# Optimization experiments

Hardware: AMD Instinct MI355X
Metric: run time of the kernel (lower is better)

The kernel has to match this reference:

```python
import jax, jax.numpy as jnp
import numpy as np

NUM_NODES = 100000
NUM_REL = 237
D = 200            # entity_out_dim_1 * nheads_GAT_1 = 100*2
C = 50             # conv_out_channels
B = 8192           # batch of (h, r, t) triples


def setup_inputs() -> dict:
    key = jax.random.key(0)
    ks = jax.random.split(key, 8)
    heads = jax.random.randint(ks[0], (B, 1), 0, NUM_NODES)
    rels = jax.random.randint(ks[1], (B, 1), 0, NUM_REL)
    tails = jax.random.randint(ks[2], (B, 1), 0, NUM_NODES)
    batch_inputs = jnp.concatenate([heads, rels, tails], axis=1).astype(jnp.int64)
    return {
        "batch_inputs": batch_inputs,
        "final_entity_embeddings": jax.random.normal(ks[3], (NUM_NODES, D), jnp.float32),
        "final_relation_embeddings": jax.random.normal(ks[4], (NUM_REL, D), jnp.float32),
        "W_ent2rel": jax.random.normal(ks[5], (NUM_REL, D, D), jnp.float32) * (1.0 / np.sqrt(D)),
        "conv_w": jax.random.normal(ks[6], (C, 3), jnp.float32) * 0.5,
        "conv_b": jnp.zeros((C,), jnp.float32),
        "fc_w": jax.random.normal(ks[7], (1, C * D), jnp.float32) * (1.0 / np.sqrt(C * D)),
        "fc_b": jnp.zeros((1,), jnp.float32),
    }


def reference(batch_inputs, final_entity_embeddings, final_relation_embeddings,
              W_ent2rel, conv_w, conv_b, fc_w, fc_b):
    h_idx, r_idx, t_idx = batch_inputs[:, 0], batch_inputs[:, 1], batch_inputs[:, 2]
    src = final_entity_embeddings[h_idx]        # [B, D]
    rel = final_relation_embeddings[r_idx]      # [B, D]
    tail = final_entity_embeddings[t_idx]       # [B, D]
    W = W_ent2rel[r_idx]                        # [B, D, D] per-edge relation transform
    # bmm([B,1,D], [B,D,D]) -> [B,1,D], nonlinearity_ent2rel = tanh
    src = jnp.tanh(jnp.einsum('bd,bde->be', src, W))
    tail = jnp.tanh(jnp.einsum('bd,bde->be', tail, W))
    # ConvKB: stack triple as length-3 sequence, Conv2d kernel (1,3) over seq
    stacked = jnp.stack([src, rel, tail], axis=1)            # [B, 3, D]
    conv = jnp.einsum('bkd,ck->bcd', stacked, conv_w) + conv_b[None, :, None]
    conv = jax.nn.relu(conv)                                  # dropout p=0.0 (eval)
    flat = conv.reshape(conv.shape[0], -1)                    # [B, C*D] (C-major, matches torch view)
    out = flat @ fc_w.T + fc_b                                # [B, 1]
    return out
```

## Files before the change

kernel.cpp:

```cpp
#include <hip/hip_runtime.h>
#include <hip/hip_bf16.h>
#include <math.h>

#define DDIM 200
#define D4   50
#define CCH  50
#define NREL 237
#define MAXE 8
#define AROWS 16
#define NT   256
#define KT   7
#define KTKG 28
#define NCOLP 208
#define OSTRIDE 204
#define PACK_UNITS (NREL * KTKG * NCOLP)

typedef __attribute__((ext_vector_type(8))) short bf16x8;
typedef __attribute__((ext_vector_type(4))) float f32x4;

__device__ __forceinline__ uint f2bf(float x) {
    __hip_bfloat16 h = __float2bfloat16(x);
    return (uint)*reinterpret_cast<ushort*>(&h);
}
__device__ __forceinline__ float fast_tanh(float x) {
    const float xc = fminf(fmaxf(x, -20.f), 20.f);
    const float e  = __expf(2.f * xc);
    return 1.f - __fdividef(2.f, e + 1.f);
}

__global__ __launch_bounds__(1024) void prep_kernel(
    const float* __restrict__ W, ushort* __restrict__ Wpk, int do_pack,
    const int* __restrict__ bi, int B, int nblk,
    int* __restrict__ perm, int* __restrict__ blk_r,
    int* __restrict__ blk_start, int* __restrict__ blk_cnt,
    int* __restrict__ eidArr)
{
    const int tid = threadIdx.x;

    if (blockIdx.x != 0) {
        if (!do_pack) return;
        const int u = (blockIdx.x - 1) * 1024 + tid;
        if (u >= PACK_UNITS) return;
        const int col  = u % NCOLP;
        const int rk   = u / NCOLP;
        const int ktkg = rk % KTKG;
        const int r    = rk / KTKG;
        const int k0   = ktkg * 8;
        uint4 pk = {0u, 0u, 0u, 0u};
        if (col < DDIM) {
            const float* base = W + (size_t)r * DDIM * DDIM + col;
            uint vv[8];
            #pragma unroll
            for (int j = 0; j < 8; ++j) {
                const int k = k0 + j;
                vv[j] = (k < DDIM) ? f2bf(base[(size_t)k * DDIM]) : 0u;
            }
            pk.x = vv[0] | (vv[1] << 16);
            pk.y = vv[2] | (vv[3] << 16);
            pk.z = vv[4] | (vv[5] << 16);
            pk.w = vv[6] | (vv[7] << 16);
        }
        *(uint4*)&Wpk[(size_t)u * 8] = pk;
        return;
    }

    __shared__ int hist[NREL];
    __shared__ int offs[NREL];
    __shared__ int wsum[16], wsum2[16];
    const int lane = tid & 63;
    const int w    = tid >> 6;

    if (tid < NREL) hist[tid] = 0;
    __syncthreads();
    for (int i = tid; i < B; i += 1024)
        atomicAdd(&hist[bi[i * 3 + 1]], 1);
    __syncthreads();

    const int v  = (tid < NREL) ? hist[tid] : 0;
    const int v2 = (tid < NREL) ? (v + MAXE - 1) / MAXE : 0;
    int s = v, s2 = v2;
    #pragma unroll
    for (int off = 1; off < 64; off <<= 1) {
        const int u  = __shfl_up(s,  off, 64);
        const int u2 = __shfl_up(s2, off, 64);
        if (lane >= off) { s += u; s2 += u2; }
    }
    if (lane == 63) { wsum[w] = s; wsum2[w] = s2; }
    __syncthreads();
    int base = 0, base2 = 0;
    for (int i = 0; i < w; ++i) { base += wsum[i]; base2 += wsum2[i]; }
    const int my_off  = base  + s  - v;
    const int my_boff = base2 + s2 - v2;
    if (tid < NREL) offs[tid] = my_off;
    __syncthreads();

    for (int i = tid; i < nblk; i += 1024) blk_cnt[i] = 0;
    if (tid < NREL && v > 0) {
        const int nb = (v + MAXE - 1) / MAXE;
        const int cb = v / nb, ext = v - cb * nb;
        int pos = my_off;
        for (int j = 0; j < nb; ++j) {
            const int c = cb + (j < ext ? 1 : 0);
            blk_r[my_boff + j]     = tid;
            blk_start[my_boff + j] = pos;
            blk_cnt[my_boff + j]   = c;
            pos += c;
        }
    }
    __syncthreads();
    for (int i = tid; i < B; i += 1024) {
        const int pos = atomicAdd(&offs[bi[i * 3 + 1]], 1);
        perm[pos] = i;
    }
    __syncthreads();
    for (int p = tid; p < B; p += 1024) {
        const int b = perm[p];
        eidArr[2 * p]     = bi[3 * b + 0];
        eidArr[2 * p + 1] = bi[3 * b + 2];
    }
}

template <bool PACKED>
__global__ __launch_bounds__(NT) void spkbgat_mfma_kernel(
    const float*  __restrict__ ent,
    const float*  __restrict__ rel_emb,
    const float*  __restrict__ W,
    const ushort* __restrict__ Wpk,
    const float*  __restrict__ conv_w,
    const float*  __restrict__ conv_b,
    const float*  __restrict__ fc_w,
    const float*  __restrict__ fc_b,
    const int*    __restrict__ perm,
    const int*    __restrict__ blk_r,
    const int*    __restrict__ blk_start,
    const int*    __restrict__ blk_cnt,
    const int*    __restrict__ eidArr,
    int nblk,
    float*        __restrict__ out)
{
    __shared__ __align__(16) ushort Ash[KTKG * AROWS * 8];
    __shared__ __align__(16) float  Osh[AROWS][OSTRIDE];
    __shared__ __align__(16) float4 rl4[D4];
    __shared__ __align__(16) float  cwb[CCH][4];

    const int tid  = threadIdx.x;
    const int w    = tid >> 6;
    const int lane = tid & 63;
    const int l16  = lane & 15;
    const int kg   = lane >> 4;

    const int bid = blockIdx.x;
    const int q = nblk >> 3, rmd = nblk & 7;
    const int xcd = bid & 7, idx = bid >> 3;
    const int gidx = (xcd < rmd ? xcd * (q + 1) : rmd * (q + 1) + (xcd - rmd) * q) + idx;

    const int cnt = blk_cnt[gidx];
    if (cnt == 0) return;

    const int r     = blk_r[gidx];
    const int start = blk_start[gidx];
    const int rows  = 2 * cnt;

    if (tid < CCH) {
        cwb[tid][0] = conv_w[tid * 3 + 0];
        cwb[tid][1] = conv_w[tid * 3 + 1];
        cwb[tid][2] = conv_w[tid * 3 + 2];
        cwb[tid][3] = conv_b[tid];
    }
    if (tid < D4) rl4[tid] = ((const float4*)rel_emb)[r * D4 + tid];

    for (int u = tid; u < KTKG * AROWS; u += NT) {
        const int row  = u & (AROWS - 1);
        const int ktkg = u >> 4;
        uint4 pk = {0u, 0u, 0u, 0u};
        if (ktkg < 25 && row < rows) {
            const int eid = eidArr[2 * start + row];
            const float* xp = ent + (size_t)eid * DDIM + ktkg * 8;
            const float4 x0 = *(const float4*)xp;
            const float4 x1 = *(const float4*)(xp + 4);
            pk.x = f2bf(x0.x) | (f2bf(x0.y) << 16);
            pk.y = f2bf(x0.z) | (f2bf(x0.w) << 16);
            pk.z = f2bf(x1.x) | (f2bf(x1.y) << 16);
            pk.w = f2bf(x1.z) | (f2bf(x1.w) << 16);
        }
        *(uint4*)&Ash[u * 8] = pk;
    }
    __syncthreads();

    const int nslots = (w == 0) ? 4 : 3;
    const float*  __restrict__ Wr = W + (size_t)r * DDIM * DDIM;
    const ushort* __restrict__ Wp0 = Wpk + (size_t)r * KTKG * NCOLP * 8
                                   + ((size_t)kg * NCOLP) * 8 + (size_t)l16 * 8;

    bf16x8 a_frag[KT];
    #pragma unroll
    for (int kt = 0; kt < KT; ++kt)
        a_frag[kt] = *(const bf16x8*)&Ash[((kt * 4 + kg) * AROWS + l16) * 8];

    f32x4 acc[4];
    #pragma unroll
    for (int s = 0; s < 4; ++s) acc[s] = (f32x4){0.f, 0.f, 0.f, 0.f};

    if (PACKED) {
        bf16x8 bcur[4], bnxt[4];
        #pragma unroll
        for (int s = 0; s < 4; ++s)
            if (s < nslots)
                bcur[s] = *(const bf16x8*)(Wp0 + (size_t)(w + 4 * s) * 16 * 8);
        #pragma unroll
        for (int kt = 0; kt < KT; ++kt) {
            if (kt + 1 < KT) {
                const ushort* pn = Wp0 + (size_t)(kt + 1) * 4 * NCOLP * 8;
                #pragma unroll
                for (int s = 0; s < 4; ++s)
                    if (s < nslots)
                        bnxt[s] = *(const bf16x8*)(pn + (size_t)(w + 4 * s) * 16 * 8);
            }
            #pragma unroll
            for (int s = 0; s < 4; ++s)
                if (s < nslots)
                    acc[s] = __builtin_amdgcn_mfma_f32_16x16x32_bf16(
                        a_frag[kt], bcur[s], acc[s], 0, 0, 0);
            #pragma unroll
            for (int s = 0; s < 4; ++s)
                if (s < nslots) bcur[s] = bnxt[s];
        }
    } else {
        for (int kt = 0; kt < KT; ++kt) {
            const int k0b = (kt * 4 + kg) * 8;
            #pragma unroll
            for (int s = 0; s < 4; ++s) {
                if (s < nslots) {
                    const int col = (w + 4 * s) * 16 + l16;
                    bf16x8 bfr;
                    #pragma unroll
                    for (int j = 0; j < 8; ++j) {
                        const int k = k0b + j;
                        const float vv = (k < DDIM && col < DDIM) ? Wr[k * DDIM + col] : 0.f;
                        bfr[j] = (short)f2bf(vv);
                    }
                    acc[s] = __builtin_amdgcn_mfma_f32_16x16x32_bf16(
                        a_frag[kt], bfr, acc[s], 0, 0, 0);
                }
            }
        }
    }

    #pragma unroll
    for (int s = 0; s < 4; ++s) {
        if (s < nslots) {
            const int gcol = (w + 4 * s) * 16 + l16;
            if (gcol < DDIM) {
                #pragma unroll
                for (int v = 0; v < 4; ++v) {
                    const int grow = kg * 4 + v;
                    if (grow < rows)
                        Osh[grow][gcol] = fast_tanh(acc[s][v]);
                }
            }
        }
    }
    __syncthreads();

    float4 sa[2] = {{0,0,0,0}, {0,0,0,0}};
    if (lane < D4) {
        const float4 rv = rl4[lane];
        float4 se[2], te[2];
        #pragma unroll
        for (int s2 = 0; s2 < 2; ++s2) {
            const int e = w + 4 * s2;
            if (e < cnt) {
                se[s2] = *(const float4*)&Osh[2 * e][4 * lane];
                te[s2] = *(const float4*)&Osh[2 * e + 1][4 * lane];
            } else {
                se[s2] = (float4){0,0,0,0};
                te[s2] = (float4){0,0,0,0};
            }
        }
        for (int c = 0; c < CCH; ++c) {
            const float4 cw  = *(const float4*)&cwb[c][0];
            const float4 fc4 = ((const float4*)fc_w)[c * D4 + lane];
            #pragma unroll
            for (int s2 = 0; s2 < 2; ++s2) {
                const float v0 = fmaf(cw.x, se[s2].x, fmaf(cw.y, rv.x, fmaf(cw.z, te[s2].x, cw.w)));
                const float v1 = fmaf(cw.x, se[s2].y, fmaf(cw.y, rv.y, fmaf(cw.z, te[s2].y, cw.w)));
                const float v2 = fmaf(cw.x, se[s2].z, fmaf(cw.y, rv.z, fmaf(cw.z, te[s2].z, cw.w)));
                const float v3 = fmaf(cw.x, se[s2].w, fmaf(cw.y, rv.w, fmaf(cw.z, te[s2].w, cw.w)));
                sa[s2].x = fmaf(fmaxf(v0, 0.f), fc4.x, sa[s2].x);
                sa[s2].y = fmaf(fmaxf(v1, 0.f), fc4.y, sa[s2].y);
                sa[s2].z = fmaf(fmaxf(v2, 0.f), fc4.z, sa[s2].z);
                sa[s2].w = fmaf(fmaxf(v3, 0.f), fc4.w, sa[s2].w);
            }
        }
    }
    #pragma unroll
    for (int s2 = 0; s2 < 2; ++s2) {
        float sum = (sa[s2].x + sa[s2].y) + (sa[s2].z + sa[s2].w);
        #pragma unroll
        for (int off = 32; off; off >>= 1)
            sum += __shfl_down(sum, off, 64);
        const int e = w + 4 * s2;
        if (lane == 0 && e < cnt)
            out[perm[start + e]] = sum + fc_b[0];
    }
}

extern "C" void kernel_launch(void* const* d_in, const int* in_sizes, int n_in,
                              void* d_out, int out_size, void* d_ws, size_t ws_size,
                              hipStream_t stream) {
    const int*   bi      = (const int*)  d_in[0];
    const float* ent     = (const float*)d_in[1];
    const float* rel_emb = (const float*)d_in[2];
    const float* W       = (const float*)d_in[3];
    const float* conv_w  = (const float*)d_in[4];
    const float* conv_b  = (const float*)d_in[5];
    const float* fc_w    = (const float*)d_in[6];
    const float* fc_b    = (const float*)d_in[7];
    float*       out     = (float*)d_out;

    const int B    = in_sizes[0] / 3;
    const int nblk = NREL + (B + MAXE - 1) / MAXE;

    int* perm      = (int*)d_ws;
    int* blk_r     = perm + B;
    int* blk_start = blk_r + nblk;
    int* blk_cnt   = blk_start + nblk;
    int* eidArr    = blk_cnt + nblk;

    const size_t meta_bytes = (size_t)(3 * B + 3 * nblk) * sizeof(int);
    const size_t pk_off     = (meta_bytes + 255) & ~(size_t)255;
    const size_t need       = pk_off + (size_t)PACK_UNITS * 16;
    const bool   use_packed = (ws_size >= need);
    ushort* Wpk = (ushort*)((char*)d_ws + pk_off);

    const int prep_blocks = 1 + (PACK_UNITS + 1023) / 1024;
    prep_kernel<<<prep_blocks, 1024, 0, stream>>>(
        W, Wpk, use_packed ? 1 : 0, bi, B, nblk,
        perm, blk_r, blk_start, blk_cnt, eidArr);

    if (use_packed) {
        spkbgat_mfma_kernel<true><<<nblk, NT, 0, stream>>>(
            ent, rel_emb, W, Wpk, conv_w, conv_b, fc_w, fc_b,
            perm, blk_r, blk_start, blk_cnt, eidArr, nblk, out);
    } else {
        spkbgat_mfma_kernel<false><<<nblk, NT, 0, stream>>>(
            ent, rel_emb, W, Wpk, conv_w, conv_b, fc_w, fc_b,
            perm, blk_r, blk_start, blk_cnt, eidArr, nblk, out);
    }
}
```

Before: 58.50 us.

## Stage W tiles in LDS for coalesced bf16 packing and fuse eid scatter

```diff
diff --git a/kernel.cpp b/kernel.cpp
--- a/kernel.cpp
+++ b/kernel.cpp
@@ -35,38 +35,51 @@
     int* __restrict__ blk_start, int* __restrict__ blk_cnt,
     int* __restrict__ eidArr)
 {
-    const int tid = threadIdx.x;
-
-    if (blockIdx.x != 0) {
-        if (!do_pack) return;
-        const int u = (blockIdx.x - 1) * 1024 + tid;
-        if (u >= PACK_UNITS) return;
-        const int col  = u % NCOLP;
-        const int rk   = u / NCOLP;
-        const int ktkg = rk % KTKG;
-        const int r    = rk / KTKG;
-        const int k0   = ktkg * 8;
-        uint4 pk = {0u, 0u, 0u, 0u};
-        if (col < DDIM) {
-            const float* base = W + (size_t)r * DDIM * DDIM + col;
-            uint vv[8];
-            #pragma unroll
-            for (int j = 0; j < 8; ++j) {
-                const int k = k0 + j;
-                vv[j] = (k < DDIM) ? f2bf(base[(size_t)k * DDIM]) : 0u;
-            }
-            pk.x = vv[0] | (vv[1] << 16);
-            pk.y = vv[2] | (vv[3] << 16);
-            pk.z = vv[4] | (vv[5] << 16);
-            pk.w = vv[6] | (vv[7] << 16);
-        }
-        *(uint4*)&Wpk[(size_t)u * 8] = pk;
-        return;
-    }
-
+    __shared__ __align__(16) float Wlds[32][DDIM];
     __shared__ int hist[NREL];
     __shared__ int offs[NREL];
     __shared__ int wsum[16], wsum2[16];
+
+    const int tid = threadIdx.x;
+
+    if (blockIdx.x != 0) {
+        if (!do_pack) return;
+        const int blk = blockIdx.x - 1;
+        const int r   = blk / KT;
+        const int kt  = blk - r * KT;
+        const int k0  = kt * 32;
+
+        for (int i = tid; i < 32 * D4; i += 1024) {
+            const int krow = i / D4;
+            const int c4   = i - krow * D4;
+            const int gk   = k0 + krow;
+            float4 v = {0.f, 0.f, 0.f, 0.f};
+            if (gk < DDIM)
+                v = *(const float4*)(W + ((size_t)r * DDIM + gk) * DDIM + 4 * c4);
+            *(float4*)&Wlds[krow][4 * c4] = v;
+        }
+        __syncthreads();
+
+        for (int u = tid; u < 4 * NCOLP; u += 1024) {
+            const int kg  = u / NCOLP;
+            const int col = u - kg * NCOLP;
+            uint4 pk = {0u, 0u, 0u, 0u};
+            if (col < DDIM) {
+                uint vv[8];
+                #pragma unroll
+                for (int j = 0; j < 8; ++j)
+                    vv[j] = f2bf(Wlds[kg * 8 + j][col]);
+                pk.x = vv[0] | (vv[1] << 16);
+                pk.y = vv[2] | (vv[3] << 16);
+                pk.z = vv[4] | (vv[5] << 16);
+                pk.w = vv[6] | (vv[7] << 16);
+            }
+            const size_t unit = ((size_t)r * KTKG + kt * 4 + kg) * NCOLP + col;
+            *(uint4*)&Wpk[unit * 8] = pk;
+        }
+        return;
+    }
+
     const int lane = tid & 63;
     const int w    = tid >> 6;
 
@@ -111,12 +124,8 @@
     for (int i = tid; i < B; i += 1024) {
         const int pos = atomicAdd(&offs[bi[i * 3 + 1]], 1);
         perm[pos] = i;
-    }
-    __syncthreads();
-    for (int p = tid; p < B; p += 1024) {
-        const int b = perm[p];
-        eidArr[2 * p]     = bi[3 * b + 0];
-        eidArr[2 * p + 1] = bi[3 * b + 2];
+        eidArr[2 * pos]     = bi[3 * i + 0];
+        eidArr[2 * pos + 1] = bi[3 * i + 2];
     }
 }
 
@@ -333,7 +342,7 @@
     const bool   use_packed = (ws_size >= need);
     ushort* Wpk = (ushort*)((char*)d_ws + pk_off);
 
-    const int prep_blocks = 1 + (PACK_UNITS + 1023) / 1024;
+    const int prep_blocks = 1 + NREL * KT;
     prep_kernel<<<prep_blocks, 1024, 0, stream>>>(
         W, Wpk, use_packed ? 1 : 0, bi, B, nblk,
         perm, blk_r, blk_start, blk_cnt, eidArr);
```

Result: faster. 54.21 us (median of 2 runs) (-7.3%).
